# Performance work log

Measured on AMD Instinct MI355X. Metric: run time of the kernel, lower is better.

## Reference

```python
import jax, jax.numpy as jnp
import numpy as np

B = 65536
H = 50          # hidden_size
L = 6           # num_layers
IN = 3          # input_size
T = 3           # seq_len


def setup_inputs() -> dict:
    key = jax.random.key(0)
    ks = jax.random.split(key, 10)
    s = 0.1  # weight init scale
    return {
        "x":     jax.random.normal(ks[0], (B, IN, T), dtype=jnp.float32),
        "h0":    jax.random.normal(ks[1], (L, B, H), dtype=jnp.float32),
        "c0":    jax.random.normal(ks[2], (L, B, H), dtype=jnp.float32),
        "w_ih0": jax.random.normal(ks[3], (4 * H, IN), dtype=jnp.float32) * s,
        "w_ih":  jax.random.normal(ks[4], (L - 1, 4 * H, H), dtype=jnp.float32) * s,
        "w_hh":  jax.random.normal(ks[5], (L, 4 * H, H), dtype=jnp.float32) * s,
        "b_ih":  jax.random.normal(ks[6], (L, 4 * H), dtype=jnp.float32) * s,
        "b_hh":  jax.random.normal(ks[7], (L, 4 * H), dtype=jnp.float32) * s,
        "fc_w":  jax.random.normal(ks[8], (1, H), dtype=jnp.float32) * s,
        "fc_b":  jax.random.normal(ks[9], (1,), dtype=jnp.float32) * s,
    }


def _lstm_layer(x_seq, h, c, w_ih, w_hh, b):
    """x_seq: [T, B, in]; returns all hidden states [T, B, H].
    PyTorch gate order: i, f, g, o."""
    def step(carry, x_t):
        h, c = carry
        gates = x_t @ w_ih.T + h @ w_hh.T + b  # [B, 4H]
        i, f, g, o = jnp.split(gates, 4, axis=-1)
        i = jax.nn.sigmoid(i)
        f = jax.nn.sigmoid(f)
        g = jnp.tanh(g)
        o = jax.nn.sigmoid(o)
        c = f * c + i * g
        h = o * jnp.tanh(c)
        return (h, c), h

    _, ys = jax.lax.scan(step, (h, c), x_seq)
    return ys


def reference(x, h0, c0, w_ih0, w_ih, w_hh, b_ih, b_hh, fc_w, fc_b):
    # original forward: input.permute(0, 2, 1) -> [B, T, IN], batch_first LSTM
    seq = jnp.transpose(x, (2, 0, 1))  # [T, B, IN] (time-major for scan)
    b = b_ih + b_hh                    # combined bias per layer [L, 4H]
    ys = _lstm_layer(seq, h0[0], c0[0], w_ih0, w_hh[0], b[0])
    for l in range(1, L):
        ys = _lstm_layer(ys, h0[l], c0[l], w_ih[l - 1], w_hh[l], b[l])
    # dropout(0.2) is identity in eval mode; take last timestep then fc
    last = ys[-1]                      # [B, H]
    return last @ fc_w.T + fc_b        # [B, 1]
```

## Files before the change

kernel.cpp:

```cpp
#include <hip/hip_runtime.h>


namespace {

constexpr int H  = 50;
constexpr int L  = 6;
constexpr int T  = 3;
constexpr int IN = 3;
constexpr int M  = 16;
constexpr int BLK = 512;
constexpr int ROWS = 72;
constexpr int NSLOT = 5;

using half8  = __attribute__((ext_vector_type(8))) _Float16;
using half2v = __attribute__((ext_vector_type(2))) _Float16;
using f32x4  = __attribute__((ext_vector_type(4))) float;

__device__ __forceinline__ float rcp_(float x) { return __builtin_amdgcn_rcpf(x); }
__device__ __forceinline__ float ex2(float x)  { return __builtin_amdgcn_exp2f(x); }

__global__ void wprep(const float* __restrict__ w_ih0, const float* __restrict__ w_ihL,
                      const float* __restrict__ w_hh,  const float* __restrict__ b_ih,
                      const float* __restrict__ b_hh,  _Float16* __restrict__ wbuf) {
  int t = blockIdx.x * 256 + threadIdx.x;
  if (t >= 384 * 64) return;
  int lam = t & 63, f = t >> 6;
  int nt = f & 15, s = (f >> 4) & 3, l = f >> 6;
  int n = nt * 16 + (lam & 15);
  int j = n >> 2, gate = n & 3, row = gate * 50 + j;
  float scale = (gate == 2) ? 2.8853900817779268f : 1.4426950408889634f;
  _Float16 o8[8];
#pragma unroll
  for (int jj = 0; jj < 8; ++jj) {
    int k = s * 32 + (lam >> 4) * 8 + jj;
    float v = 0.f;
    if (j < H) {
      if (s < 2) {
        int ksz = (l == 0) ? IN : H;
        if (k < ksz) v = (l == 0) ? w_ih0[row * IN + k]
                                  : w_ihL[((size_t)(l - 1) * 200 + row) * H + k];
      } else {
        int kh = k - 64;
        if (kh < H)        v = w_hh[((size_t)l * 200 + row) * H + kh];
        else if (kh == 63) v = b_ih[l * 200 + row] + b_hh[l * 200 + row];
      }
    }
    o8[jj] = (_Float16)(v * scale);
  }
  ((half8*)wbuf)[t] = *(half8*)o8;
}

__global__ __launch_bounds__(BLK, 8)
void lstm_mfma(const float* __restrict__ x,   const float* __restrict__ h0,
               const float* __restrict__ c0,  const float* __restrict__ fc_w,
               const float* __restrict__ fc_b, const _Float16* __restrict__ wbuf,
               float* __restrict__ out, int B) {
  const int tid = threadIdx.x;
  const int lam = tid & 63;
  const int q   = lam >> 4;
  const int lm  = lam & 15;
  const int bbase = blockIdx.x * M;
  const int ng  = __builtin_amdgcn_readfirstlane(tid >> 6);
  const int ntp = __builtin_amdgcn_readfirstlane((ng + blockIdx.x) & 7);
  const int ntg0 = 2 * ntp, ntg1 = 2 * ntp + 1;
  const bool live0 = (ntg0 <= 12);
  const bool live1 = (ntg1 <= 12);
  const int j0 = 4 * ntg0 + q, j1 = 4 * ntg1 + q;

  __shared__ __align__(16) _Float16 ys[NSLOT][M][ROWS];

  if (tid < NSLOT * M) {
    _Float16* row = &ys[0][0][0] + (size_t)tid * ROWS;
#pragma unroll
    for (int z = 0; z < 6; ++z)
      *(unsigned int*)(row + 50 + 2 * z) = 0u;
    half2v pb; pb[0] = (_Float16)0.f; pb[1] = (_Float16)1.f;
    *(half2v*)(row + 62) = pb;
  }
  if (tid < T * M) {
    const int t = tid >> 4, m = tid & 15;
    const float* xs = x + (size_t)(bbase + m) * (IN * T) + t;
    _Float16* row = &ys[2 + t][m][0];
    half2v p0; p0[0] = (_Float16)xs[0]; p0[1] = (_Float16)xs[3];
    half2v p1; p1[0] = (_Float16)xs[6]; p1[1] = (_Float16)0.f;
    *(half2v*)(row)     = p0;
    *(half2v*)(row + 2) = p1;
#pragma unroll
    for (int z = 0; z < 7; ++z)
      *(unsigned long long*)(row + 4 + 4 * z) = 0ull;
  }
  __syncthreads();

  float cc[2];
  f32x4 xa[2];
  half8 W[2][4];
  const f32x4 z4 = {0.f, 0.f, 0.f, 0.f};

  const _Float16* rbase = &ys[0][lm][q * 8];

#pragma unroll
  for (int l = 0; l < L; ++l) {
    const int sh0 = (4 * l) % 5;
    const int s1 = (sh0 + 1) % 5;
    const int s2 = (sh0 + 2) % 5;
    const int s3 = (sh0 + 3) % 5;
    const int s4 = (sh0 + 4) % 5;

    if (live0) {
      cc[0] = (j0 < H) ? c0[((size_t)l * B + bbase + lm) * H + j0] : 0.f;
      cc[1] = (live1 && j1 < H) ? c0[((size_t)l * B + bbase + lm) * H + j1] : 0.f;
#pragma unroll
      for (int s = 0; s < 4; ++s)
        W[0][s] = ((const half8*)wbuf)[((l * 4 + s) * 16 + ntg0) * 64 + lam];
      if (live1)
#pragma unroll
        for (int s = 0; s < 4; ++s)
          W[1][s] = ((const half8*)wbuf)[((l * 4 + s) * 16 + ntg1) * 64 + lam];
      {
        half8 Xf = *(const half8*)(rbase + s2 * (M * ROWS));
        xa[0] = __builtin_amdgcn_mfma_f32_16x16x32_f16(W[0][0], Xf, z4, 0, 0, 0);
        if (live1)
          xa[1] = __builtin_amdgcn_mfma_f32_16x16x32_f16(W[1][0], Xf, z4, 0, 0, 0);
        if (l > 0) {
          half8 Xg = *(const half8*)(rbase + s2 * (M * ROWS) + 32);
          xa[0] = __builtin_amdgcn_mfma_f32_16x16x32_f16(W[0][1], Xg, xa[0], 0, 0, 0);
          if (live1)
            xa[1] = __builtin_amdgcn_mfma_f32_16x16x32_f16(W[1][1], Xg, xa[1], 0, 0, 0);
        }
      }
    }
    {
      const int mg = tid >> 5, kpl = tid & 31;
      if (kpl < 25) {
        float2 v = *(const float2*)(h0 + ((size_t)l * B + bbase + mg) * H + 2 * kpl);
        half2v pv; pv[0] = (_Float16)v.x; pv[1] = (_Float16)v.y;
        *(half2v*)(&ys[sh0][mg][2 * kpl]) = pv;
      }
    }
    __syncthreads();

#pragma unroll
    for (int t = 0; t < T; ++t) {
      const int shs = (t == 0) ? sh0 : ((t == 1) ? s1 : s2);
      const int sot = (t == 0) ? s1  : ((t == 1) ? s2 : s3);
      const int sxt = (t == 0) ? s3  : s4;
      if (live0) {
#pragma unroll
        for (int s = 0; s < 2; ++s) {
          half8 Hf = *(const half8*)(rbase + shs * (M * ROWS) + s * 32);
          xa[0] = __builtin_amdgcn_mfma_f32_16x16x32_f16(W[0][2 + s], Hf, xa[0], 0, 0, 0);
          if (live1)
            xa[1] = __builtin_amdgcn_mfma_f32_16x16x32_f16(W[1][2 + s], Hf, xa[1], 0, 0, 0);
        }
        {
          const float ig = rcp_(1.f + ex2(-xa[0][0]));
          const float fg = rcp_(1.f + ex2(-xa[0][1]));
          const float gg = 2.f * rcp_(1.f + ex2(-xa[0][2])) - 1.f;
          const float og = rcp_(1.f + ex2(-xa[0][3]));
          const float cv = fg * cc[0] + ig * gg;
          cc[0] = cv;
          const float tc = 2.f * rcp_(1.f + ex2(-2.8853900817779268f * cv)) - 1.f;
          if (j0 < H)
            ys[sot][lm][j0] = (_Float16)(og * tc);
        }
        if (live1) {
          const float ig = rcp_(1.f + ex2(-xa[1][0]));
          const float fg = rcp_(1.f + ex2(-xa[1][1]));
          const float gg = 2.f * rcp_(1.f + ex2(-xa[1][2])) - 1.f;
          const float og = rcp_(1.f + ex2(-xa[1][3]));
          const float cv = fg * cc[1] + ig * gg;
          cc[1] = cv;
          const float tc = 2.f * rcp_(1.f + ex2(-2.8853900817779268f * cv)) - 1.f;
          if (j1 < H)
            ys[sot][lm][j1] = (_Float16)(og * tc);
        }
        if (t < T - 1) {
          half8 Xf = *(const half8*)(rbase + sxt * (M * ROWS));
          xa[0] = __builtin_amdgcn_mfma_f32_16x16x32_f16(W[0][0], Xf, z4, 0, 0, 0);
          if (live1)
            xa[1] = __builtin_amdgcn_mfma_f32_16x16x32_f16(W[1][0], Xf, z4, 0, 0, 0);
          if (l > 0) {
            half8 Xg = *(const half8*)(rbase + sxt * (M * ROWS) + 32);
            xa[0] = __builtin_amdgcn_mfma_f32_16x16x32_f16(W[0][1], Xg, xa[0], 0, 0, 0);
            if (live1)
              xa[1] = __builtin_amdgcn_mfma_f32_16x16x32_f16(W[1][1], Xg, xa[1], 0, 0, 0);
          }
        }
      }
      __syncthreads();
    }
  }

  if (tid < 8 * M) {
    int m = tid >> 3, strip = tid & 7;
    float part = 0.f;
#pragma unroll
    for (int jj = 0; jj < 7; ++jj) {
      int jf = strip + 8 * jj;
      if (jf < H) part += fc_w[jf] * (float)ys[3][m][jf];
    }
    part += __shfl_xor(part, 4);
    part += __shfl_xor(part, 2);
    part += __shfl_xor(part, 1);
    if (strip == 0) out[bbase + m] = part + fc_b[0];
  }
}

}

extern "C" void kernel_launch(void* const* d_in, const int* in_sizes, int n_in,
                              void* d_out, int out_size, void* d_ws, size_t ws_size,
                              hipStream_t stream) {
  const float* x     = (const float*)d_in[0];
  const float* h0    = (const float*)d_in[1];
  const float* c0    = (const float*)d_in[2];
  const float* w_ih0 = (const float*)d_in[3];
  const float* w_ih  = (const float*)d_in[4];
  const float* w_hh  = (const float*)d_in[5];
  const float* b_ih  = (const float*)d_in[6];
  const float* b_hh  = (const float*)d_in[7];
  const float* fc_w  = (const float*)d_in[8];
  const float* fc_b  = (const float*)d_in[9];
  float* out         = (float*)d_out;

  const int B = in_sizes[0] / (IN * T);
  _Float16* wbuf = (_Float16*)d_ws;

  wprep<<<(384 * 64 + 255) / 256, 256, 0, stream>>>(w_ih0, w_ih, w_hh, b_ih, b_hh, wbuf);
  lstm_mfma<<<B / M, BLK, 0, stream>>>(x, h0, c0, fc_w, fc_b, wbuf, out, B);
}
```

Baseline: 279.2 us.

## Process 32 batch rows per block and hoist input projections out of recurrence

```diff
diff --git a/kernel.cpp b/kernel.cpp
--- a/kernel.cpp
+++ b/kernel.cpp
@@ -7,10 +7,11 @@
 constexpr int L  = 6;
 constexpr int T  = 3;
 constexpr int IN = 3;
-constexpr int M  = 16;
-constexpr int BLK = 512;
+constexpr int M  = 32;
+constexpr int BLK = 1024;
 constexpr int ROWS = 72;
 constexpr int NSLOT = 5;
+constexpr int SLOT = M * ROWS;
 
 using half8  = __attribute__((ext_vector_type(8))) _Float16;
 using half2v = __attribute__((ext_vector_type(2))) _Float16;
@@ -60,12 +61,10 @@
   const int q   = lam >> 4;
   const int lm  = lam & 15;
   const int bbase = blockIdx.x * M;
-  const int ng  = __builtin_amdgcn_readfirstlane(tid >> 6);
-  const int ntp = __builtin_amdgcn_readfirstlane((ng + blockIdx.x) & 7);
-  const int ntg0 = 2 * ntp, ntg1 = 2 * ntp + 1;
-  const bool live0 = (ntg0 <= 12);
-  const bool live1 = (ntg1 <= 12);
-  const int j0 = 4 * ntg0 + q, j1 = 4 * ntg1 + q;
+  const int w   = __builtin_amdgcn_readfirstlane(tid >> 6);
+  const int ntg = __builtin_amdgcn_readfirstlane((w + blockIdx.x) & 15);
+  const bool live = (ntg <= 12);
+  const int j = 4 * ntg + q;
 
   __shared__ __align__(16) _Float16 ys[NSLOT][M][ROWS];
 
@@ -78,7 +77,7 @@
     *(half2v*)(row + 62) = pb;
   }
   if (tid < T * M) {
-    const int t = tid >> 4, m = tid & 15;
+    const int t = tid >> 5, m = tid & 31;
     const float* xs = x + (size_t)(bbase + m) * (IN * T) + t;
     _Float16* row = &ys[2 + t][m][0];
     half2v p0; p0[0] = (_Float16)xs[0]; p0[1] = (_Float16)xs[3];
@@ -92,11 +91,47 @@
   __syncthreads();
 
   float cc[2];
-  f32x4 xa[2];
-  half8 W[2][4];
+  f32x4 xa0[2], xa1[2], xa2[2];
+  half8 W4[4];
   const f32x4 z4 = {0.f, 0.f, 0.f, 0.f};
 
   const _Float16* rbase = &ys[0][lm][q * 8];
+
+#define XPART(acc, slot) do {                                                  \
+    half8 X0a = *(const half8*)(rbase + (slot) * SLOT);                        \
+    half8 X0b = *(const half8*)(rbase + (slot) * SLOT + 16 * ROWS);            \
+    acc[0] = __builtin_amdgcn_mfma_f32_16x16x32_f16(W4[0], X0a, z4, 0, 0, 0);  \
+    acc[1] = __builtin_amdgcn_mfma_f32_16x16x32_f16(W4[0], X0b, z4, 0, 0, 0);  \
+    if (l > 0) {                       \
+      half8 X1a = *(const half8*)(rbase + (slot) * SLOT + 32);                 \
+      half8 X1b = *(const half8*)(rbase + (slot) * SLOT + 16 * ROWS + 32);     \
+      acc[0] = __builtin_amdgcn_mfma_f32_16x16x32_f16(W4[1], X1a, acc[0], 0, 0, 0); \
+      acc[1] = __builtin_amdgcn_mfma_f32_16x16x32_f16(W4[1], X1b, acc[1], 0, 0, 0); \
+    }                                                                          \
+  } while (0)
+#define ACT1(acc, mt, sot) do {                                                \
+    const float ig = rcp_(1.f + ex2(-acc[mt][0]));                             \
+    const float fg = rcp_(1.f + ex2(-acc[mt][1]));                             \
+    const float gg = 2.f * rcp_(1.f + ex2(-acc[mt][2])) - 1.f;                 \
+    const float og = rcp_(1.f + ex2(-acc[mt][3]));                             \
+    const float cv = fg * cc[mt] + ig * gg;                                    \
+    cc[mt] = cv;                                                               \
+    const float tc = 2.f * rcp_(1.f + ex2(-2.8853900817779268f * cv)) - 1.f;   \
+    if (j < H)                                 \
+      ys[sot][(mt) * 16 + lm][j] = (_Float16)(og * tc);                        \
+  } while (0)
+#define STEP(acc, shs, sot) do {                                               \
+    half8 Hf0a = *(const half8*)(rbase + (shs) * SLOT);                        \
+    half8 Hf0b = *(const half8*)(rbase + (shs) * SLOT + 16 * ROWS);            \
+    acc[0] = __builtin_amdgcn_mfma_f32_16x16x32_f16(W4[2], Hf0a, acc[0], 0, 0, 0); \
+    acc[1] = __builtin_amdgcn_mfma_f32_16x16x32_f16(W4[2], Hf0b, acc[1], 0, 0, 0); \
+    half8 Hf1a = *(const half8*)(rbase + (shs) * SLOT + 32);                   \
+    half8 Hf1b = *(const half8*)(rbase + (shs) * SLOT + 16 * ROWS + 32);       \
+    acc[0] = __builtin_amdgcn_mfma_f32_16x16x32_f16(W4[3], Hf1a, acc[0], 0, 0, 0); \
+    acc[1] = __builtin_amdgcn_mfma_f32_16x16x32_f16(W4[3], Hf1b, acc[1], 0, 0, 0); \
+    ACT1(acc, 0, sot);                                                         \
+    ACT1(acc, 1, sot);                                                         \
+  } while (0)
 
 #pragma unroll
   for (int l = 0; l < L; ++l) {
@@ -106,28 +141,15 @@
     const int s3 = (sh0 + 3) % 5;
     const int s4 = (sh0 + 4) % 5;
 
-    if (live0) {
-      cc[0] = (j0 < H) ? c0[((size_t)l * B + bbase + lm) * H + j0] : 0.f;
-      cc[1] = (live1 && j1 < H) ? c0[((size_t)l * B + bbase + lm) * H + j1] : 0.f;
+    if (live) {
+      cc[0] = (j < H) ? c0[((size_t)l * B + bbase + lm) * H + j] : 0.f;
+      cc[1] = (j < H) ? c0[((size_t)l * B + bbase + 16 + lm) * H + j] : 0.f;
 #pragma unroll
       for (int s = 0; s < 4; ++s)
-        W[0][s] = ((const half8*)wbuf)[((l * 4 + s) * 16 + ntg0) * 64 + lam];
-      if (live1)
-#pragma unroll
-        for (int s = 0; s < 4; ++s)
-          W[1][s] = ((const half8*)wbuf)[((l * 4 + s) * 16 + ntg1) * 64 + lam];
-      {
-        half8 Xf = *(const half8*)(rbase + s2 * (M * ROWS));
-        xa[0] = __builtin_amdgcn_mfma_f32_16x16x32_f16(W[0][0], Xf, z4, 0, 0, 0);
-        if (live1)
-          xa[1] = __builtin_amdgcn_mfma_f32_16x16x32_f16(W[1][0], Xf, z4, 0, 0, 0);
-        if (l > 0) {
-          half8 Xg = *(const half8*)(rbase + s2 * (M * ROWS) + 32);
-          xa[0] = __builtin_amdgcn_mfma_f32_16x16x32_f16(W[0][1], Xg, xa[0], 0, 0, 0);
-          if (live1)
-            xa[1] = __builtin_amdgcn_mfma_f32_16x16x32_f16(W[1][1], Xg, xa[1], 0, 0, 0);
-        }
-      }
+        W4[s] = ((const half8*)wbuf)[((l * 4 + s) * 16 + ntg) * 64 + lam];
+      XPART(xa0, s2);
+      XPART(xa1, s3);
+      XPART(xa2, s4);
     }
     {
       const int mg = tid >> 5, kpl = tid & 31;
@@ -139,57 +161,16 @@
     }
     __syncthreads();
 
-#pragma unroll
-    for (int t = 0; t < T; ++t) {
-      const int shs = (t == 0) ? sh0 : ((t == 1) ? s1 : s2);
-      const int sot = (t == 0) ? s1  : ((t == 1) ? s2 : s3);
-      const int sxt = (t == 0) ? s3  : s4;
-      if (live0) {
-#pragma unroll
-        for (int s = 0; s < 2; ++s) {
-          half8 Hf = *(const half8*)(rbase + shs * (M * ROWS) + s * 32);
-          xa[0] = __builtin_amdgcn_mfma_f32_16x16x32_f16(W[0][2 + s], Hf, xa[0], 0, 0, 0);
-          if (live1)
-            xa[1] = __builtin_amdgcn_mfma_f32_16x16x32_f16(W[1][2 + s], Hf, xa[1], 0, 0, 0);
-        }
-        {
-          const float ig = rcp_(1.f + ex2(-xa[0][0]));
-          const float fg = rcp_(1.f + ex2(-xa[0][1]));
-          const float gg = 2.f * rcp_(1.f + ex2(-xa[0][2])) - 1.f;
-          const float og = rcp_(1.f + ex2(-xa[0][3]));
-          const float cv = fg * cc[0] + ig * gg;
-          cc[0] = cv;
-          const float tc = 2.f * rcp_(1.f + ex2(-2.8853900817779268f * cv)) - 1.f;
-          if (j0 < H)
-            ys[sot][lm][j0] = (_Float16)(og * tc);
-        }
-        if (live1) {
-          const float ig = rcp_(1.f + ex2(-xa[1][0]));
-          const float fg = rcp_(1.f + ex2(-xa[1][1]));
-          const float gg = 2.f * rcp_(1.f + ex2(-xa[1][2])) - 1.f;
-          const float og = rcp_(1.f + ex2(-xa[1][3]));
-          const float cv = fg * cc[1] + ig * gg;
-          cc[1] = cv;
-          const float tc = 2.f * rcp_(1.f + ex2(-2.8853900817779268f * cv)) - 1.f;
-          if (j1 < H)
-            ys[sot][lm][j1] = (_Float16)(og * tc);
-        }
-        if (t < T - 1) {
-          half8 Xf = *(const half8*)(rbase + sxt * (M * ROWS));
-          xa[0] = __builtin_amdgcn_mfma_f32_16x16x32_f16(W[0][0], Xf, z4, 0, 0, 0);
-          if (live1)
-            xa[1] = __builtin_amdgcn_mfma_f32_16x16x32_f16(W[1][0], Xf, z4, 0, 0, 0);
-          if (l > 0) {
-            half8 Xg = *(const half8*)(rbase + sxt * (M * ROWS) + 32);
-            xa[0] = __builtin_amdgcn_mfma_f32_16x16x32_f16(W[0][1], Xg, xa[0], 0, 0, 0);
-            if (live1)
-              xa[1] = __builtin_amdgcn_mfma_f32_16x16x32_f16(W[1][1], Xg, xa[1], 0, 0, 0);
-          }
-        }
-      }
-      __syncthreads();
-    }
-  }
+    if (live) STEP(xa0, sh0, s1);
+    __syncthreads();
+    if (live) STEP(xa1, s1, s2);
+    __syncthreads();
+    if (live) STEP(xa2, s2, s3);
+    __syncthreads();
+  }
+#undef XPART
+#undef ACT1
+#undef STEP
 
   if (tid < 8 * M) {
     int m = tid >> 3, strip = tid & 7;
```

Measured after the change: 280.2 us. About the same (+0.4%).
